# Kernel optimization log

Hardware: AMD Instinct MI355X
Metric: run time of the kernel (lower is better)

The kernel has to match this reference:

```python
import jax, jax.numpy as jnp
import numpy as np

DIM = 1024
N_HEADS = 16
HEAD_DIM = DIM // N_HEADS
LORA_DIM = 16
B, T = 4, 1024


def _rope(x):
    # x: [B, H, T, D] with D even; rotate first/second halves (torch impl style)
    D = x.shape[-1]
    half = D // 2
    theta = 1.0 / (10000.0 ** (jnp.arange(0, D, 2, dtype=jnp.float32) / D))  # [D/2]
    pos = jnp.arange(x.shape[-2], dtype=jnp.float32)                         # [T]
    pt = pos[:, None] * theta[None, :]                                       # [T, D/2]
    sin, cos = jnp.sin(pt), jnp.cos(pt)
    xr, xi = x[..., :half], x[..., half:]
    return jnp.concatenate([xr * cos - xi * sin, xr * sin + xi * cos], axis=-1)


def setup_inputs() -> dict:
    key = jax.random.key(0)
    ks = jax.random.split(key, 16)
    def n(k, shape, std=0.02):
        return jax.random.normal(k, shape, jnp.float32) * std
    return {
        "x": jax.random.normal(ks[0], (B, T, DIM), jnp.float32),
        "q_w": n(ks[1], (DIM, DIM)),
        "k_w": n(ks[2], (DIM, DIM)),
        "v_w": n(ks[3], (DIM, DIM)),
        "q_a": n(ks[4], (LORA_DIM, DIM), 0.001),
        "q_b": n(ks[5], (DIM, LORA_DIM), 0.001),
        "q_l": jax.random.normal(ks[6], (DIM,), jnp.float32),
        "k_a": n(ks[7], (LORA_DIM, DIM), 0.001),
        "k_b": n(ks[8], (DIM, LORA_DIM), 0.001),
        "k_l": jax.random.normal(ks[9], (DIM,), jnp.float32),
        "v_a": n(ks[10], (LORA_DIM, DIM), 0.001),
        "v_b": n(ks[11], (DIM, LORA_DIM), 0.001),
        "v_l": jax.random.normal(ks[12], (DIM,), jnp.float32),
        "proj_w": n(ks[13], (DIM, DIM)),
        "proj_b": n(ks[14], (DIM,)),
    }


def reference(x, q_w, k_w, v_w, q_a, q_b, q_l, k_a, k_b, k_l,
              v_a, v_b, v_l, proj_w, proj_b):
    Bb, Tt, C = x.shape
    # token shift: xx[t] = x[t-1], xx[0] = 0 (ZeroPad2d((0,0,1,-1)))
    xx = jnp.pad(x, ((0, 0), (1, 0), (0, 0)))[:, :Tt]
    xxx = xx - x

    def lora(a, b, lam):
        return lam + jnp.tanh(x @ a.T) @ b.T  # [B,T,C]

    q = (x + xxx * lora(q_a, q_b, q_l)) @ q_w.T
    k = (x + xxx * lora(k_a, k_b, k_l)) @ k_w.T
    v = (x + xxx * lora(v_a, v_b, v_l)) @ v_w.T

    def split_heads(t):
        return t.reshape(Bb, Tt, N_HEADS, HEAD_DIM).transpose(0, 2, 1, 3)  # [B,H,T,D]

    q = _rope(split_heads(q))
    k = _rope(split_heads(k))
    v = split_heads(v)

    scale = 1.0 / np.sqrt(HEAD_DIM).astype(np.float32)
    scores = jnp.einsum('bhqd,bhkd->bhqk', q, k) * scale
    causal = jnp.tril(jnp.ones((Tt, Tt), dtype=bool))
    scores = jnp.where(causal, scores, jnp.float32(-1e30))
    att = jax.nn.softmax(scores, axis=-1)
    out = jnp.einsum('bhqk,bhkd->bhqd', att, v)
    out = out.transpose(0, 2, 1, 3).reshape(Bb, Tt, C)
    return out @ proj_w.T + proj_b
```

## Files before the change

### kernel.cpp

```cpp
#include <hip/hip_runtime.h>
#include <hip/hip_bf16.h>

typedef __hip_bfloat16 bf16;
typedef __attribute__((ext_vector_type(8))) short bf16x8;
typedef __attribute__((ext_vector_type(4))) float f32x4;

typedef const __attribute__((address_space(1))) unsigned int* gp_t;
typedef __attribute__((address_space(3))) unsigned int* lp_t;

__device__ __forceinline__ bf16 tobf(float f) { return __float2bfloat16(f); }
__device__ __forceinline__ float tof(bf16 h) { return __bfloat162float(h); }

__device__ __forceinline__ short bfbits(float f) {
    bf16 h = __float2bfloat16(f);
    return *reinterpret_cast<short*>(&h);
}
__device__ __forceinline__ bf16x8 pack8(float4 a, float4 b) {
    bf16x8 r;
    r[0] = bfbits(a.x); r[1] = bfbits(a.y); r[2] = bfbits(a.z); r[3] = bfbits(a.w);
    r[4] = bfbits(b.x); r[5] = bfbits(b.y); r[6] = bfbits(b.z); r[7] = bfbits(b.w);
    return r;
}

__device__ __forceinline__ void gload_lds16(const void* g, void* l) {
    __builtin_amdgcn_global_load_lds((gp_t)g, (lp_t)l, 16, 0, 0);
}

__global__ __launch_bounds__(256) void convert_w(const float* qw, const float* kw,
                                                 const float* vw, const float* pw,
                                                 bf16* dst) {
    int m = blockIdx.y;
    const float* src = m == 0 ? qw : (m == 1 ? kw : (m == 2 ? vw : pw));
    bf16* d = dst + (size_t)m * (1u << 20);
    int i = (blockIdx.x * 256 + threadIdx.x) * 4;
    float4 f = *(const float4*)(src + i);
    d[i + 0] = tobf(f.x);
    d[i + 1] = tobf(f.y);
    d[i + 2] = tobf(f.z);
    d[i + 3] = tobf(f.w);
}

__global__ __launch_bounds__(256) void lora_gate_fused(
    const float* x,
    const float* qa, const float* ka, const float* va,
    const float* qbw, const float* ql,
    const float* kbw, const float* kl,
    const float* vbw, const float* vl,
    bf16* xqo, bf16* xko, bf16* xvo) {
    const int XS = 1028;
    int row0 = blockIdx.x * 16;
    int t0 = row0 & 1023;
    int tid = threadIdx.x;
    int wave = tid >> 6, lane = tid & 63;
    int quad = lane >> 4, l16 = lane & 15;

    __shared__ float sx[17 * 1028];
    __shared__ float sT[16 * 48];

    {
        int prow = (row0 == 0) ? 0 : row0 - 1;
        for (int i = 0; i < 17; ++i) {
            int grow = (i == 0) ? prow : row0 + i - 1;
            gload_lds16(x + (size_t)grow * 1024 + wave * 256 + lane * 4,
                        &sx[i * XS + wave * 256]);
        }
    }
    __syncthreads();

    if (wave < 3) {
        const float* am = wave == 0 ? qa : (wave == 1 ? ka : va);
        f32x4 acc = (f32x4){0.f, 0.f, 0.f, 0.f};
#pragma unroll 4
        for (int k0 = 0; k0 < 1024; k0 += 32) {
            const float* xs = &sx[(1 + l16) * XS + k0 + quad * 8];
            bf16x8 af = pack8(*(const float4*)xs, *(const float4*)(xs + 4));
            const float* as = am + (size_t)l16 * 1024 + k0 + quad * 8;
            bf16x8 bf_ = pack8(*(const float4*)as, *(const float4*)(as + 4));
            acc = __builtin_amdgcn_mfma_f32_16x16x32_bf16(af, bf_, acc, 0, 0, 0);
        }
#pragma unroll
        for (int r = 0; r < 4; ++r)
            sT[(quad * 4 + r) * 48 + wave * 16 + l16] = tanhf(acc[r]);
    }
    __syncthreads();

#pragma unroll
    for (int u = 0; u < 4; ++u) {
        int d = tid + u * 256;
        float qbv[16], kbv[16], vbv[16];
#pragma unroll
        for (int p = 0; p < 4; ++p) {
            *(float4*)&qbv[p * 4] = *(const float4*)(qbw + (size_t)d * 16 + p * 4);
            *(float4*)&kbv[p * 4] = *(const float4*)(kbw + (size_t)d * 16 + p * 4);
            *(float4*)&vbv[p * 4] = *(const float4*)(vbw + (size_t)d * 16 + p * 4);
        }
        float qlv = ql[d], klv = kl[d], vlv = vl[d];
        float xp = (t0 == 0) ? 0.f : sx[0 * XS + d];
        for (int rr = 0; rr < 16; ++rr) {
            float xc = sx[(rr + 1) * XS + d];
            float dx = xp - xc;
            float gq = qlv, gk = klv, gv = vlv;
#pragma unroll
            for (int j = 0; j < 16; ++j) {
                gq += sT[rr * 48 + j] * qbv[j];
                gk += sT[rr * 48 + 16 + j] * kbv[j];
                gv += sT[rr * 48 + 32 + j] * vbv[j];
            }
            size_t o = (size_t)(row0 + rr) * 1024 + d;
            xqo[o] = tobf(xc + dx * gq);
            xko[o] = tobf(xc + dx * gk);
            xvo[o] = tobf(xc + dx * gv);
            xp = xc;
        }
    }
}

__global__ __launch_bounds__(256) void gemm128(
    const bf16* A0, const bf16* A1, const bf16* A2,
    const bf16* W0, const bf16* W1, const bf16* W2,
    bf16* C0, bf16* C1, bf16* C2,
    const float* bias, float* outF, int proj) {
    const int K = 1024;
    int bz = blockIdx.z;
    const bf16* A = bz == 0 ? A0 : (bz == 1 ? A1 : A2);
    const bf16* W = bz == 0 ? W0 : (bz == 1 ? W1 : W2);
    bf16* C = bz == 0 ? C0 : (bz == 1 ? C1 : C2);
    int m0 = blockIdx.y * 128, n0 = blockIdx.x * 128;

    __shared__ alignas(16) bf16 sA[128 * 32];
    __shared__ alignas(16) bf16 sB[128 * 32];

    int wave = threadIdx.x >> 6, lane = threadIdx.x & 63;
    int quad = lane >> 4, l16 = lane & 15;

    f32x4 acc[4][4];
#pragma unroll
    for (int i = 0; i < 4; i++)
#pragma unroll
        for (int j = 0; j < 4; j++) acc[i][j] = (f32x4){0.f, 0.f, 0.f, 0.f};

    int srow = wave * 16 + (lane >> 2);
    int scol = (lane & 3) * 8;

    for (int k0 = 0; k0 < K; k0 += 32) {
        __syncthreads();
#pragma unroll
        for (int p = 0; p < 2; p++) {
            int row = p * 64 + srow;
            gload_lds16(A + (size_t)(m0 + row) * K + k0 + scol, &sA[(p * 64 + wave * 16) * 32]);
            gload_lds16(W + (size_t)(n0 + row) * K + k0 + scol, &sB[(p * 64 + wave * 16) * 32]);
        }
        __syncthreads();
        int mw = (wave >> 1) * 64, nw = (wave & 1) * 64;
        bf16x8 af[4], bfr[4];
#pragma unroll
        for (int f = 0; f < 4; f++) {
            af[f] = *(const bf16x8*)&sA[(mw + f * 16 + l16) * 32 + quad * 8];
            bfr[f] = *(const bf16x8*)&sB[(nw + f * 16 + l16) * 32 + quad * 8];
        }
#pragma unroll
        for (int i = 0; i < 4; i++)
#pragma unroll
            for (int j = 0; j < 4; j++)
                acc[i][j] = __builtin_amdgcn_mfma_f32_16x16x32_bf16(af[i], bfr[j], acc[i][j], 0, 0, 0);
    }

    int mw = (wave >> 1) * 64, nw = (wave & 1) * 64;
#pragma unroll
    for (int i = 0; i < 4; i++) {
        int mrow = m0 + mw + i * 16 + quad * 4;
#pragma unroll
        for (int j = 0; j < 4; j++) {
            int col = n0 + nw + j * 16 + l16;
            if (proj) {
                float bv = bias[col];
#pragma unroll
                for (int r = 0; r < 4; r++)
                    outF[(size_t)(mrow + r) * 1024 + col] = acc[i][j][r] + bv;
            } else {
#pragma unroll
                for (int r = 0; r < 4; r++)
                    C[(size_t)(mrow + r) * 1024 + col] = tobf(acc[i][j][r]);
            }
        }
    }
}

__global__ __launch_bounds__(256) void rope_transform(
    const bf16* q, const bf16* k, const bf16* v,
    bf16* Qh, bf16* Kh, bf16* Vt) {
    int bh = blockIdx.x, tblk = blockIdx.y;
    int b = bh >> 4, h = bh & 15;
    int t0 = tblk * 64;
    int tid = threadIdx.x;

    int i0 = (tid & 7) * 4;
#pragma unroll
    for (int pp = 0; pp < 2; ++pp) {
        int t = t0 + pp * 32 + (tid >> 3);
        size_t gin = ((size_t)(b * 1024 + t)) * 1024 + h * 64;
        size_t gout = ((size_t)(bh * 1024 + t)) * 64;
        float c[4], s[4];
#pragma unroll
        for (int u = 0; u < 4; ++u) {
            int i = i0 + u;
            float theta = __expf(-(float)i * (9.210340371976184f / 32.0f));
            sincosf((float)t * theta, &s[u], &c[u]);
        }
        float xr[4], xi[4];
#pragma unroll
        for (int u = 0; u < 4; u++) { xr[u] = tof(q[gin + i0 + u]); xi[u] = tof(q[gin + 32 + i0 + u]); }
#pragma unroll
        for (int u = 0; u < 4; u++) {
            Qh[gout + i0 + u]      = tobf((xr[u] * c[u] - xi[u] * s[u]) * 0.125f);
            Qh[gout + 32 + i0 + u] = tobf((xr[u] * s[u] + xi[u] * c[u]) * 0.125f);
        }
#pragma unroll
        for (int u = 0; u < 4; u++) { xr[u] = tof(k[gin + i0 + u]); xi[u] = tof(k[gin + 32 + i0 + u]); }
#pragma unroll
        for (int u = 0; u < 4; u++) {
            Kh[gout + i0 + u]      = tobf(xr[u] * c[u] - xi[u] * s[u]);
            Kh[gout + 32 + i0 + u] = tobf(xr[u] * s[u] + xi[u] * c[u]);
        }
    }

    __shared__ bf16 sv[64 * 65];
    {
        int r = tid >> 2;
        int c0 = (tid & 3) * 16;
        size_t g = ((size_t)(b * 1024 + t0 + r)) * 1024 + h * 64 + c0;
#pragma unroll
        for (int u = 0; u < 16; u++) sv[(c0 + u) * 65 + r] = v[g + u];
    }
    __syncthreads();
    {
        int d = tid >> 2;
        int tc = (tid & 3) * 16;
        size_t g = ((size_t)(bh * 64 + d)) * 1024 + t0 + tc;
#pragma unroll
        for (int u = 0; u < 16; u++) Vt[g + u] = sv[d * 65 + tc + u];
    }
}

__global__ __launch_bounds__(256) void attention(const bf16* Qh, const bf16* Kh,
                                                 const bf16* Vt, bf16* attn) {
    int gid = blockIdx.x;
    int qblk = 15 - (gid >> 6);
    int bh = (((gid >> 3) & 7) << 3) | (gid & 7);
    int b = bh >> 4, h = bh & 15;
    int wave = threadIdx.x >> 6, lane = threadIdx.x & 63;
    int quad = lane >> 4, l16 = lane & 15;
    int m7 = l16 & 7;

    const bf16* Qb = Qh + (size_t)bh * 1024 * 64;
    const bf16* Kb = Kh + (size_t)bh * 1024 * 64;
    const bf16* Vb = Vt + (size_t)bh * 64 * 1024;

    __shared__ alignas(16) bf16 sK[2][64 * 64];
    __shared__ alignas(16) bf16 sV[2][64 * 64];
    __shared__ alignas(16) bf16 sP[4][16 * 64];

    int srow = lane >> 3;
    int scol = ((lane & 7) ^ srow) * 8;

    auto stage = [&](int kt, int bufi) {
#pragma unroll
        for (int p = 0; p < 2; p++) {
            int rbase = p * 32 + wave * 8;
            gload_lds16(Kb + (size_t)(kt * 64 + rbase + srow) * 64 + scol, &sK[bufi][rbase * 64]);
            gload_lds16(Vb + (size_t)(rbase + srow) * 1024 + kt * 64 + scol, &sV[bufi][rbase * 64]);
        }
    };

    int qrow0 = qblk * 64 + wave * 16;
    bf16x8 aq0 = *(const bf16x8*)&Qb[(size_t)(qrow0 + l16) * 64 + quad * 8];
    bf16x8 aq1 = *(const bf16x8*)&Qb[(size_t)(qrow0 + l16) * 64 + quad * 8 + 32];

    f32x4 o[4];
#pragma unroll
    for (int nt = 0; nt < 4; nt++) o[nt] = (f32x4){0.f, 0.f, 0.f, 0.f};
    float mrow[4], lrow[4];
#pragma unroll
    for (int r = 0; r < 4; r++) { mrow[r] = -3.0e38f; lrow[r] = 0.f; }

    stage(0, 0);

    int buf = 0;
    for (int kt = 0; kt <= qblk; ++kt, buf ^= 1) {
        __syncthreads();
        if (kt < qblk) stage(kt + 1, buf ^ 1);

        f32x4 S[4];
#pragma unroll
        for (int j = 0; j < 4; j++) {
            int row = j * 16 + l16;
            bf16x8 bk0 = *(const bf16x8*)&sK[buf][row * 64 + ((quad ^ m7) * 8)];
            bf16x8 bk1 = *(const bf16x8*)&sK[buf][row * 64 + (((quad + 4) ^ m7) * 8)];
            f32x4 z = __builtin_amdgcn_mfma_f32_16x16x32_bf16(aq0, bk0, (f32x4){0.f, 0.f, 0.f, 0.f}, 0, 0, 0);
            S[j] = __builtin_amdgcn_mfma_f32_16x16x32_bf16(aq1, bk1, z, 0, 0, 0);
        }
        if (kt == qblk) {
#pragma unroll
            for (int j = 0; j < 4; j++) {
                int key = kt * 64 + j * 16 + l16;
#pragma unroll
                for (int r = 0; r < 4; r++) {
                    int qr = qrow0 + quad * 4 + r;
                    if (key > qr) S[j][r] = -3.0e38f;
                }
            }
        }
        float alpha[4];
#pragma unroll
        for (int r = 0; r < 4; r++) {
            float vmax = fmaxf(fmaxf(S[0][r], S[1][r]), fmaxf(S[2][r], S[3][r]));
            vmax = fmaxf(vmax, __shfl_xor(vmax, 1));
            vmax = fmaxf(vmax, __shfl_xor(vmax, 2));
            vmax = fmaxf(vmax, __shfl_xor(vmax, 4));
            vmax = fmaxf(vmax, __shfl_xor(vmax, 8));
            float mn = fmaxf(mrow[r], vmax);
            alpha[r] = __expf(mrow[r] - mn);
            mrow[r] = mn;
        }
        float rs[4] = {0.f, 0.f, 0.f, 0.f};
#pragma unroll
        for (int j = 0; j < 4; j++)
#pragma unroll
            for (int r = 0; r < 4; r++) {
                float p = __expf(S[j][r] - mrow[r]);
                S[j][r] = p;
                rs[r] += p;
            }
#pragma unroll
        for (int r = 0; r < 4; r++) {
            float v = rs[r];
            v += __shfl_xor(v, 1);
            v += __shfl_xor(v, 2);
            v += __shfl_xor(v, 4);
            v += __shfl_xor(v, 8);
            lrow[r] = lrow[r] * alpha[r] + v;
        }
#pragma unroll
        for (int nt = 0; nt < 4; nt++)
#pragma unroll
            for (int r = 0; r < 4; r++) o[nt][r] *= alpha[r];

#pragma unroll
        for (int j = 0; j < 4; j++) {
            int c = j * 2 + (l16 >> 3);
#pragma unroll
            for (int r = 0; r < 4; r++) {
                int prow = quad * 4 + r;
                sP[wave][prow * 64 + ((c ^ (prow & 7)) * 8) + m7] = tobf(S[j][r]);
            }
        }
        asm volatile("s_waitcnt lgkmcnt(0)" ::: "memory");
        bf16x8 ap0 = *(const bf16x8*)&sP[wave][l16 * 64 + ((quad ^ m7) * 8)];
        bf16x8 ap1 = *(const bf16x8*)&sP[wave][l16 * 64 + (((quad + 4) ^ m7) * 8)];
#pragma unroll
        for (int nt = 0; nt < 4; nt++) {
            int row = nt * 16 + l16;
            bf16x8 bv0 = *(const bf16x8*)&sV[buf][row * 64 + ((quad ^ m7) * 8)];
            bf16x8 bv1 = *(const bf16x8*)&sV[buf][row * 64 + (((quad + 4) ^ m7) * 8)];
            o[nt] = __builtin_amdgcn_mfma_f32_16x16x32_bf16(ap0, bv0, o[nt], 0, 0, 0);
            o[nt] = __builtin_amdgcn_mfma_f32_16x16x32_bf16(ap1, bv1, o[nt], 0, 0, 0);
        }
    }

    float invl[4];
#pragma unroll
    for (int r = 0; r < 4; r++) invl[r] = 1.0f / lrow[r];
#pragma unroll
    for (int nt = 0; nt < 4; nt++)
#pragma unroll
        for (int r = 0; r < 4; r++) {
            int t = qrow0 + quad * 4 + r;
            int col = h * 64 + nt * 16 + l16;
            attn[(size_t)(b * 1024 + t) * 1024 + col] = tobf(o[nt][r] * invl[r]);
        }
}

extern "C" void kernel_launch(void* const* d_in, const int* in_sizes, int n_in,
                              void* d_out, int out_size, void* d_ws, size_t ws_size,
                              hipStream_t stream) {
    const float* x = (const float*)d_in[0];
    const float* qw = (const float*)d_in[1];
    const float* kw = (const float*)d_in[2];
    const float* vw = (const float*)d_in[3];
    const float* qa = (const float*)d_in[4];
    const float* qb = (const float*)d_in[5];
    const float* ql = (const float*)d_in[6];
    const float* ka = (const float*)d_in[7];
    const float* kb = (const float*)d_in[8];
    const float* kl = (const float*)d_in[9];
    const float* va = (const float*)d_in[10];
    const float* vb = (const float*)d_in[11];
    const float* vl = (const float*)d_in[12];
    const float* pw = (const float*)d_in[13];
    const float* pb = (const float*)d_in[14];
    float* out = (float*)d_out;

    char* ws = (char*)d_ws;
    const size_t MB = 1024 * 1024;
    bf16* wqb = (bf16*)ws;
    bf16* wkb = wqb + 1048576;
    bf16* wvb = wkb + 1048576;
    bf16* wpb = wvb + 1048576;
    bf16* xqb = (bf16*)(ws + 8 * MB);
    bf16* xkb = xqb + 4194304;
    bf16* xvb = xkb + 4194304;
    bf16* qm = (bf16*)(ws + 32 * MB);
    bf16* km = qm + 4194304;
    bf16* vm = km + 4194304;
    bf16* Qh = xqb;
    bf16* Kh = xkb;
    bf16* Vt = xvb;
    bf16* attn = qm;

    convert_w<<<dim3(1024, 4), 256, 0, stream>>>(qw, kw, vw, pw, wqb);
    lora_gate_fused<<<256, 256, 0, stream>>>(x, qa, ka, va, qb, ql, kb, kl, vb, vl,
                                             xqb, xkb, xvb);
    gemm128<<<dim3(8, 32, 3), 256, 0, stream>>>(xqb, xkb, xvb, wqb, wkb, wvb, qm, km, vm,
                                                nullptr, nullptr, 0);
    rope_transform<<<dim3(64, 16), 256, 0, stream>>>(qm, km, vm, Qh, Kh, Vt);
    attention<<<1024, 256, 0, stream>>>(Qh, Kh, Vt, attn);
    gemm128<<<dim3(8, 32, 1), 256, 0, stream>>>(attn, nullptr, nullptr, wpb, nullptr, nullptr,
                                                nullptr, nullptr, nullptr, pb, out, 1);
}
```

Baseline: 234.8 us.

## Deepen GEMM K-tile to 64 with XOR-swizzled LDS and XCD-aware block mapping

The QKV and projection GEMM now loads 64-wide K slices per iteration instead of 32, which halves the number of barrier pairs. Global-to-LDS columns are XOR-swizzled by row to avoid LDS bank conflicts on the fragment reads. The grid is flattened to 1D and remapped so the blocks on each XCD (blockIdx & 7) share the same M rows, to improve L2 reuse. LDS use doubles to 32KB per block, which may lower occupancy.

```diff
diff --git a/kernel.cpp b/kernel.cpp
--- a/kernel.cpp
+++ b/kernel.cpp
@@ -119,68 +119,79 @@
     const bf16* A0, const bf16* A1, const bf16* A2,
     const bf16* W0, const bf16* W1, const bf16* W2,
     bf16* C0, bf16* C1, bf16* C2,
-    const float* bias, float* outF, int proj) {
+    const float* bias, float* outF, int proj, int zcnt) {
     const int K = 1024;
-    int bz = blockIdx.z;
+    int ppx = (zcnt * 32) >> 3;
+    int xcd = blockIdx.x & 7;
+    int j = blockIdx.x >> 3;
+    int pair = xcd * ppx + (j >> 3);
+    int n0 = (j & 7) * 128;
+    int bz = pair >> 5;
+    int m0 = (pair & 31) * 128;
+
     const bf16* A = bz == 0 ? A0 : (bz == 1 ? A1 : A2);
     const bf16* W = bz == 0 ? W0 : (bz == 1 ? W1 : W2);
     bf16* C = bz == 0 ? C0 : (bz == 1 ? C1 : C2);
-    int m0 = blockIdx.y * 128, n0 = blockIdx.x * 128;
-
-    __shared__ alignas(16) bf16 sA[128 * 32];
-    __shared__ alignas(16) bf16 sB[128 * 32];
+
+    __shared__ alignas(16) bf16 sA[128 * 64];
+    __shared__ alignas(16) bf16 sB[128 * 64];
 
     int wave = threadIdx.x >> 6, lane = threadIdx.x & 63;
     int quad = lane >> 4, l16 = lane & 15;
+    int m7 = l16 & 7;
 
     f32x4 acc[4][4];
 #pragma unroll
     for (int i = 0; i < 4; i++)
 #pragma unroll
-        for (int j = 0; j < 4; j++) acc[i][j] = (f32x4){0.f, 0.f, 0.f, 0.f};
-
-    int srow = wave * 16 + (lane >> 2);
-    int scol = (lane & 3) * 8;
-
-    for (int k0 = 0; k0 < K; k0 += 32) {
+        for (int j2 = 0; j2 < 4; j2++) acc[i][j2] = (f32x4){0.f, 0.f, 0.f, 0.f};
+
+    int srow = lane >> 3;
+    int scol = ((lane & 7) ^ srow) * 8;
+
+    int mw = (wave >> 1) * 64, nw = (wave & 1) * 64;
+
+    for (int k0 = 0; k0 < K; k0 += 64) {
         __syncthreads();
 #pragma unroll
-        for (int p = 0; p < 2; p++) {
-            int row = p * 64 + srow;
-            gload_lds16(A + (size_t)(m0 + row) * K + k0 + scol, &sA[(p * 64 + wave * 16) * 32]);
-            gload_lds16(W + (size_t)(n0 + row) * K + k0 + scol, &sB[(p * 64 + wave * 16) * 32]);
+        for (int p = 0; p < 4; p++) {
+            int rbase = wave * 32 + p * 8;
+            gload_lds16(A + (size_t)(m0 + rbase + srow) * K + k0 + scol, &sA[rbase * 64]);
+            gload_lds16(W + (size_t)(n0 + rbase + srow) * K + k0 + scol, &sB[rbase * 64]);
         }
         __syncthreads();
-        int mw = (wave >> 1) * 64, nw = (wave & 1) * 64;
-        bf16x8 af[4], bfr[4];
-#pragma unroll
-        for (int f = 0; f < 4; f++) {
-            af[f] = *(const bf16x8*)&sA[(mw + f * 16 + l16) * 32 + quad * 8];
-            bfr[f] = *(const bf16x8*)&sB[(nw + f * 16 + l16) * 32 + quad * 8];
-        }
-#pragma unroll
-        for (int i = 0; i < 4; i++)
-#pragma unroll
-            for (int j = 0; j < 4; j++)
-                acc[i][j] = __builtin_amdgcn_mfma_f32_16x16x32_bf16(af[i], bfr[j], acc[i][j], 0, 0, 0);
-    }
-
-    int mw = (wave >> 1) * 64, nw = (wave & 1) * 64;
+#pragma unroll
+        for (int ks = 0; ks < 2; ks++) {
+            bf16x8 af[4], bfr[4];
+#pragma unroll
+            for (int f = 0; f < 4; f++) {
+                int c = ((quad + ks * 4) ^ m7) * 8;
+                af[f] = *(const bf16x8*)&sA[(mw + f * 16 + l16) * 64 + c];
+                bfr[f] = *(const bf16x8*)&sB[(nw + f * 16 + l16) * 64 + c];
+            }
+#pragma unroll
+            for (int i = 0; i < 4; i++)
+#pragma unroll
+                for (int j2 = 0; j2 < 4; j2++)
+                    acc[i][j2] = __builtin_amdgcn_mfma_f32_16x16x32_bf16(af[i], bfr[j2], acc[i][j2], 0, 0, 0);
+        }
+    }
+
 #pragma unroll
     for (int i = 0; i < 4; i++) {
         int mrow = m0 + mw + i * 16 + quad * 4;
 #pragma unroll
-        for (int j = 0; j < 4; j++) {
-            int col = n0 + nw + j * 16 + l16;
+        for (int j2 = 0; j2 < 4; j2++) {
+            int col = n0 + nw + j2 * 16 + l16;
             if (proj) {
                 float bv = bias[col];
 #pragma unroll
                 for (int r = 0; r < 4; r++)
-                    outF[(size_t)(mrow + r) * 1024 + col] = acc[i][j][r] + bv;
+                    outF[(size_t)(mrow + r) * 1024 + col] = acc[i][j2][r] + bv;
             } else {
 #pragma unroll
                 for (int r = 0; r < 4; r++)
-                    C[(size_t)(mrow + r) * 1024 + col] = tobf(acc[i][j][r]);
+                    C[(size_t)(mrow + r) * 1024 + col] = tobf(acc[i][j2][r]);
             }
         }
     }
@@ -420,10 +431,10 @@
     convert_w<<<dim3(1024, 4), 256, 0, stream>>>(qw, kw, vw, pw, wqb);
     lora_gate_fused<<<256, 256, 0, stream>>>(x, qa, ka, va, qb, ql, kb, kl, vb, vl,
                                              xqb, xkb, xvb);
-    gemm128<<<dim3(8, 32, 3), 256, 0, stream>>>(xqb, xkb, xvb, wqb, wkb, wvb, qm, km, vm,
-                                                nullptr, nullptr, 0);
+    gemm128<<<768, 256, 0, stream>>>(xqb, xkb, xvb, wqb, wkb, wvb, qm, km, vm,
+                                     nullptr, nullptr, 0, 3);
     rope_transform<<<dim3(64, 16), 256, 0, stream>>>(qm, km, vm, Qh, Kh, Vt);
     attention<<<1024, 256, 0, stream>>>(Qh, Kh, Vt, attn);
-    gemm128<<<dim3(8, 32, 1), 256, 0, stream>>>(attn, nullptr, nullptr, wpb, nullptr, nullptr,
-                                                nullptr, nullptr, nullptr, pb, out, 1);
-}
+    gemm128<<<256, 256, 0, stream>>>(attn, nullptr, nullptr, wpb, nullptr, nullptr,
+                                     nullptr, nullptr, nullptr, pb, out, 1, 1);
+}
```

Result: no change. 234.8 us (+0.0%).
